# Optimization experiments

Measured on AMD Instinct MI355X. Metric: run time of the kernel, lower is better.

## Reference

```python
import jax, jax.numpy as jnp
import numpy as np

B, S, D, H, F = 4, 2048, 1024, 16, 4096
HD = D // H
NEG = -2.0 ** 32
EPS = 1e-5


def _gelu(x):
    return x * 0.5 * (1.0 + jax.scipy.special.erf(x / jnp.sqrt(2.0).astype(x.dtype)))


def _layernorm(x, scale, offset):
    mu = jnp.mean(x, axis=-1, keepdims=True)
    var = jnp.mean(jnp.square(x - mu), axis=-1, keepdims=True)
    return (x - mu) * jax.lax.rsqrt(var + EPS) * scale + offset


def setup_inputs() -> dict:
    key = jax.random.key(0)
    ks = jax.random.split(key, 12)
    s = 0.02
    return {
        "x": jax.random.normal(ks[0], (B, S, D), jnp.float32),
        "mask": jnp.zeros((B, S), jnp.int32),  # 1 = masked-out (padding)
        "Wq": jax.random.normal(ks[1], (D, D), jnp.float32) * s,
        "bq": jnp.zeros((D,), jnp.float32),
        "Wk": jax.random.normal(ks[2], (D, D), jnp.float32) * s,
        "bk": jnp.zeros((D,), jnp.float32),
        "Wv": jax.random.normal(ks[3], (D, D), jnp.float32) * s,
        "bv": jnp.zeros((D,), jnp.float32),
        "Wo": jax.random.normal(ks[4], (D, D), jnp.float32) * s,
        "bo": jnp.zeros((D,), jnp.float32),
        "ln1_s": jnp.ones((D,), jnp.float32),
        "ln1_b": jnp.zeros((D,), jnp.float32),
        "W1": jax.random.normal(ks[5], (D, F), jnp.float32) * s,
        "b1": jnp.zeros((F,), jnp.float32),
        "W2": jax.random.normal(ks[6], (F, D), jnp.float32) * s,
        "b2": jnp.zeros((D,), jnp.float32),
        "ln2_s": jnp.ones((D,), jnp.float32),
        "ln2_b": jnp.zeros((D,), jnp.float32),
    }


def reference(x, mask, Wq, bq, Wk, bk, Wv, bv, Wo, bo, ln1_s, ln1_b,
              W1, b1, W2, b2, ln2_s, ln2_b):
    b, s, d = x.shape
    q = (x @ Wq + bq).reshape(b, s, H, HD)
    k = (x @ Wk + bk).reshape(b, s, H, HD)
    v = (x @ Wv + bv).reshape(b, s, H, HD)
    logits = jnp.einsum('btnh,bsnh->bnts', q, k) / jnp.sqrt(jnp.float32(HD))
    logits = logits + (mask.astype(jnp.float32) * NEG)[:, None, None, :]
    attn = jax.nn.softmax(logits, axis=-1)
    ctx = jnp.einsum('bsnh,bnts->btnh', v, attn).reshape(b, s, d)
    attn_out = ctx @ Wo + bo
    h = _layernorm(attn_out + x, ln1_s, ln1_b)
    mlp = _gelu(h @ W1 + b1) @ W2 + b2
    return _layernorm(mlp + h, ln2_s, ln2_b)
```

## Files before the change

kernel.cpp:

```cpp
#include <hip/hip_runtime.h>
#include <hip/hip_bf16.h>

typedef __attribute__((ext_vector_type(8))) short short8;
typedef __attribute__((ext_vector_type(4))) short s16x4;
typedef __attribute__((ext_vector_type(4))) float f32x4;
typedef unsigned short u16;

#define DEV __device__ __forceinline__
#define MFMA32(a, b, c) __builtin_amdgcn_mfma_f32_16x16x32_bf16(a, b, c, 0, 0, 0)
#define MFMA16(a, b, c) __builtin_amdgcn_mfma_f32_16x16x16bf16_1k(a, b, c, 0, 0, 0)

DEV u16 f2b(float f) {
    __hip_bfloat16 h = __float2bfloat16(f);
    return __builtin_bit_cast(unsigned short, h);
}

DEV float max3f(float a, float b, float c) {
    float d;
    asm("v_max3_f32 %0, %1, %2, %3" : "=v"(d) : "v"(a), "v"(b), "v"(c));
    return d;
}

DEV void gl_lds16(const u16* g, u16* l) {
    __builtin_amdgcn_global_load_lds((const unsigned int*)g, (unsigned int*)l, 16, 0, 0);
}

__global__ __launch_bounds__(256) void cast_bf16(const float* __restrict__ in, u16* __restrict__ out, int n) {
    int i = (blockIdx.x * 256 + threadIdx.x) * 4;
    if (i < n) {
        float4 v = *(const float4*)(in + i);
        ushort4 o;
        o.x = f2b(v.x); o.y = f2b(v.y); o.z = f2b(v.z); o.w = f2b(v.w);
        *(ushort4*)(out + i) = o;
    }
}

__global__ __launch_bounds__(256) void transpose_cast(const float* __restrict__ in, u16* __restrict__ out,
                                                      int R, int C) {
    __shared__ float t[32][33];
    int bx = blockIdx.x * 32;
    int by = blockIdx.y * 32;
    int tx = threadIdx.x, ty = threadIdx.y;
#pragma unroll
    for (int i = 0; i < 32; i += 8) t[ty + i][tx] = in[(size_t)(by + ty + i) * C + bx + tx];
    __syncthreads();
#pragma unroll
    for (int i = 0; i < 32; i += 8) out[(size_t)(bx + ty + i) * R + by + tx] = f2b(t[tx][ty + i]);
}

__global__ __launch_bounds__(256) void pack_bias(const float* __restrict__ bq, const float* __restrict__ bk,
                                                 const float* __restrict__ bv, const float* __restrict__ bo,
                                                 const float* __restrict__ b1, const float* __restrict__ b2,
                                                 float* __restrict__ out) {
    int i = blockIdx.x * 256 + threadIdx.x;
    if (i >= 9216) return;
    float v;
    if (i < 1024) v = bq[i];
    else if (i < 2048) v = bk[i - 1024];
    else if (i < 3072) v = bv[i - 2048];
    else if (i < 4096) v = bo[i - 3072];
    else if (i < 8192) v = b1[i - 4096];
    else v = b2[i - 8192];
    out[i] = v;
}

template <bool GELU, bool BF16OUT, bool RESID>
__global__ __launch_bounds__(256) void gemm_bt(const u16* __restrict__ A, const u16* __restrict__ B,
                                               const float* __restrict__ bias, float* __restrict__ cf,
                                               u16* __restrict__ cb, const float* __restrict__ res,
                                               int M, int N, int K) {
    __shared__ __align__(16) u16 As[128 * 32];
    __shared__ __align__(16) u16 Bs[128 * 32];
    const int tid = threadIdx.x;
    const int wid = tid >> 6, lane = tid & 63;
    const int wr = wid >> 1, wc = wid & 1;
    const int m0 = blockIdx.x * 128, n0 = blockIdx.y * 128;
    const int r16 = lane & 15, g = lane >> 4;
    const int lrow = lane >> 2, lk = (lane & 3) * 8;

    f32x4 acc[4][4];
#pragma unroll
    for (int i = 0; i < 4; i++)
#pragma unroll
        for (int j = 0; j < 4; j++) acc[i][j] = (f32x4){0.f, 0.f, 0.f, 0.f};

    const u16* ga = A + (size_t)(m0 + wid * 32 + lrow) * K + lk;
    const u16* gb = B + (size_t)(n0 + wid * 32 + lrow) * K + lk;
    u16* lA0 = &As[(wid * 32) * 32];
    u16* lA1 = &As[(wid * 32 + 16) * 32];
    u16* lB0 = &Bs[(wid * 32) * 32];
    u16* lB1 = &Bs[(wid * 32 + 16) * 32];

    for (int kt = 0; kt < K; kt += 32) {
        gl_lds16(ga + kt, lA0);
        gl_lds16(ga + (size_t)16 * K + kt, lA1);
        gl_lds16(gb + kt, lB0);
        gl_lds16(gb + (size_t)16 * K + kt, lB1);
        __syncthreads();
        short8 af[4], bfr[4];
#pragma unroll
        for (int i = 0; i < 4; i++) af[i] = *(const short8*)&As[(wr * 64 + i * 16 + r16) * 32 + g * 8];
#pragma unroll
        for (int j = 0; j < 4; j++) bfr[j] = *(const short8*)&Bs[(wc * 64 + j * 16 + r16) * 32 + g * 8];
#pragma unroll
        for (int i = 0; i < 4; i++)
#pragma unroll
            for (int j = 0; j < 4; j++) acc[i][j] = MFMA32(af[i], bfr[j], acc[i][j]);
        __syncthreads();
    }

#pragma unroll
    for (int i = 0; i < 4; i++) {
#pragma unroll
        for (int j = 0; j < 4; j++) {
#pragma unroll
            for (int r = 0; r < 4; r++) {
                int row = m0 + wr * 64 + i * 16 + g * 4 + r;
                int col = n0 + wc * 64 + j * 16 + r16;
                float v = acc[i][j][r] + bias[col];
                if (RESID) v += res[(size_t)row * N + col];
                if (GELU) v = 0.5f * v * (1.0f + erff(v * 0.70710678118654752f));
                if (BF16OUT) cb[(size_t)row * N + col] = f2b(v);
                else cf[(size_t)row * N + col] = v;
            }
        }
    }
}

__global__ __launch_bounds__(256) void attn_kernel(const u16* __restrict__ qkv, const int* __restrict__ mask,
                                                   u16* __restrict__ ctx) {
    const int tid = threadIdx.x, wid = tid >> 6, lane = tid & 63;
    const int r16 = lane & 15, g = lane >> 4;
    const int h = blockIdx.y, b = blockIdx.z;
    const size_t baserow = (size_t)b * 2048;
    const int q0 = blockIdx.x * 64;

    __shared__ __align__(16) u16 Ks[64 * 64];
    __shared__ __align__(16) u16 Vs[64 * 64];
    __shared__ unsigned tflags_sh;

    const float SCALE = 0.18033688011112042f;
    const float MNEG = -6.196328018e9f;
    const s16x4 ONES = {(short)0x3F80, (short)0x3F80, (short)0x3F80, (short)0x3F80};

    short8 qf0, qf1;
    {
        const u16* qp = qkv + (baserow + q0 + wid * 16 + r16) * 3072 + h * 64 + g * 8;
        qf0 = *(const short8*)qp;
        qf1 = *(const short8*)(qp + 32);
    }

    if (tid == 0) tflags_sh = 0;
    __syncthreads();
    for (int r = 0; r < 8; ++r) {
        int v = mask[baserow + r * 256 + tid];
        unsigned long long bal = __ballot(v != 0);
        if (bal != 0 && lane == 0) atomicOr(&tflags_sh, 1u << (r * 4 + wid));
    }

    const int L = lane;
    const int kchunk = (L & 7) ^ (L >> 3);
    const u16* kg0 = qkv + (baserow + wid * 16 + (L >> 3)) * 3072 + 1024 + h * 64 + kchunk * 8;
    const u16* kg1 = kg0 + (size_t)8 * 3072;
    u16* kl0 = &Ks[wid * 1024];
    u16* kl1 = &Ks[wid * 1024 + 512];
    const u16* vg0 = qkv + (baserow + wid * 16 + ((L & 31) >> 1)) * 3072 + 2048 + h * 64
                     + ((L >> 5) * 16 + (L & 1) * 8);
    const u16* vg1 = vg0 + 32;
    u16* vl0 = &Vs[wid * 1024];
    u16* vl1 = &Vs[wid * 1024 + 512];
    const unsigned vaddr = (unsigned)(unsigned long long)&Vs[0] + (unsigned)(r16 * 2 + g * 128);

    __syncthreads();
    const unsigned tfl = tflags_sh;

    f32x4 Ot[4];
#pragma unroll
    for (int dt = 0; dt < 4; dt++) Ot[dt] = (f32x4){0.f, 0.f, 0.f, 0.f};
    f32x4 Osum = (f32x4){0.f, 0.f, 0.f, 0.f};
    float mrun = -1e30f;

    for (int t = 0; t < 32; ++t) {
        const int kt = t * 64;
        const size_t go = (size_t)kt * 3072;
        gl_lds16(kg0 + go, kl0);
        gl_lds16(kg1 + go, kl1);
        gl_lds16(vg0 + go, vl0);
        gl_lds16(vg1 + go, vl1);
        __syncthreads();

        f32x4 z[4];
        __builtin_amdgcn_s_setprio(1);
#pragma unroll
        for (int tt = 0; tt < 4; tt++) {
            const int row = tt * 16 + r16;
            const int swz = row & 7;
            short8 a0 = *(const short8*)&Ks[row * 64 + ((g ^ swz) * 8)];
            short8 a1 = *(const short8*)&Ks[row * 64 + (((4 + g) ^ swz) * 8)];
            f32x4 zz = (f32x4){0.f, 0.f, 0.f, 0.f};
            zz = MFMA32(a0, qf0, zz);
            zz = MFMA32(a1, qf1, zz);
            z[tt] = zz;
        }
        __builtin_amdgcn_s_setprio(0);

        float m0 = max3f(z[0][0], z[0][1], z[0][2]);
        float m1 = max3f(z[0][3], z[1][0], z[1][1]);
        float m2 = max3f(z[1][2], z[1][3], z[2][0]);
        float m3 = max3f(z[2][1], z[2][2], z[2][3]);
        float m4 = max3f(z[3][0], z[3][1], z[3][2]);
        float zmax = fmaxf(max3f(m0, m1, m2), max3f(m3, m4, z[3][3]));
        zmax = fmaxf(zmax, __shfl_xor(zmax, 16));
        zmax = fmaxf(zmax, __shfl_xor(zmax, 32));
        float pmax = zmax * SCALE;

        if (!__all(pmax - mrun <= 11.5f)) {
            float mnew = fmaxf(mrun, pmax);
            float alpha = exp2f(mrun - mnew);
            mrun = mnew;
            Osum *= alpha;
#pragma unroll
            for (int dt = 0; dt < 4; dt++) Ot[dt] *= alpha;
        }

        s16x4 pb[4];
        const float negm = -mrun;
        if (__builtin_expect((tfl >> t) & 1u, 0)) {
            const int* mrow = mask + baserow + kt;
#pragma unroll
            for (int tt = 0; tt < 4; tt++) {
                float p[4];
#pragma unroll
                for (int j = 0; j < 4; j++) {
                    float mbj = mrow[tt * 16 + g * 4 + j] ? MNEG : 0.0f;
                    p[j] = exp2f(__builtin_fmaf(z[tt][j], SCALE, mbj + negm));
                }
                unsigned lo, hi;
                asm("v_cvt_pk_bf16_f32 %0, %1, %2" : "=v"(lo) : "v"(p[0]), "v"(p[1]));
                asm("v_cvt_pk_bf16_f32 %0, %1, %2" : "=v"(hi) : "v"(p[2]), "v"(p[3]));
                uint2 u; u.x = lo; u.y = hi;
                pb[tt] = __builtin_bit_cast(s16x4, u);
            }
        } else {
#pragma unroll
            for (int tt = 0; tt < 4; tt++) {
                float p0 = exp2f(__builtin_fmaf(z[tt][0], SCALE, negm));
                float p1 = exp2f(__builtin_fmaf(z[tt][1], SCALE, negm));
                float p2 = exp2f(__builtin_fmaf(z[tt][2], SCALE, negm));
                float p3 = exp2f(__builtin_fmaf(z[tt][3], SCALE, negm));
                unsigned lo, hi;
                asm("v_cvt_pk_bf16_f32 %0, %1, %2" : "=v"(lo) : "v"(p0), "v"(p1));
                asm("v_cvt_pk_bf16_f32 %0, %1, %2" : "=v"(hi) : "v"(p2), "v"(p3));
                uint2 u; u.x = lo; u.y = hi;
                pb[tt] = __builtin_bit_cast(s16x4, u);
            }
        }

        s16x4 vf[4][4];
#pragma unroll
        for (int tt = 0; tt < 4; tt++)
#pragma unroll
            for (int dt = 0; dt < 4; dt++)
                asm volatile("ds_read_b64_tr_b16 %0, %1"
                             : "=v"(vf[tt][dt])
                             : "v"(vaddr + (unsigned)((tt * 4 + dt) * 512)));
        asm volatile("s_waitcnt lgkmcnt(0)" ::: "memory");
        __builtin_amdgcn_sched_barrier(0);
        __builtin_amdgcn_s_setprio(1);
#pragma unroll
        for (int tt = 0; tt < 4; tt++) {
#pragma unroll
            for (int dt = 0; dt < 4; dt++) Ot[dt] = MFMA16(vf[tt][dt], pb[tt], Ot[dt]);
            Osum = MFMA16(ONES, pb[tt], Osum);
        }
        __builtin_amdgcn_s_setprio(0);
        __syncthreads();
    }

    const float rl = 1.0f / Osum[0];
    u16* cp = ctx + (baserow + q0 + wid * 16 + r16) * 1024 + h * 64 + g * 4;
#pragma unroll
    for (int dt = 0; dt < 4; dt++) {
        ushort4 o4;
        o4.x = f2b(Ot[dt][0] * rl);
        o4.y = f2b(Ot[dt][1] * rl);
        o4.z = f2b(Ot[dt][2] * rl);
        o4.w = f2b(Ot[dt][3] * rl);
        *(ushort4*)(cp + dt * 16) = o4;
    }
}

__global__ __launch_bounds__(256) void ln_kernel(const float* __restrict__ a, const float* __restrict__ res,
                                                 const float* __restrict__ gamma, const float* __restrict__ beta,
                                                 float* __restrict__ outf, u16* __restrict__ outb) {
    const int row = blockIdx.x, tid = threadIdx.x;
    const size_t base = (size_t)row * 1024 + tid * 4;
    float4 va = *(const float4*)(a + base);
    float x0 = va.x, x1 = va.y, x2 = va.z, x3 = va.w;
    if (res) {
        float4 vr = *(const float4*)(res + base);
        x0 += vr.x; x1 += vr.y; x2 += vr.z; x3 += vr.w;
    }
    float s = x0 + x1 + x2 + x3;
    float ss = x0 * x0 + x1 * x1 + x2 * x2 + x3 * x3;
#pragma unroll
    for (int m = 1; m < 64; m <<= 1) { s += __shfl_xor(s, m, 64); ss += __shfl_xor(ss, m, 64); }
    __shared__ float red[8];
    if ((tid & 63) == 0) { red[tid >> 6] = s; red[4 + (tid >> 6)] = ss; }
    __syncthreads();
    s = red[0] + red[1] + red[2] + red[3];
    ss = red[4] + red[5] + red[6] + red[7];
    float mu = s * (1.0f / 1024.0f);
    float var = ss * (1.0f / 1024.0f) - mu * mu;
    float rstd = rsqrtf(var + 1e-5f);
    float4 g4 = *(const float4*)(gamma + tid * 4);
    float4 b4 = *(const float4*)(beta + tid * 4);
    float y0 = (x0 - mu) * rstd * g4.x + b4.x;
    float y1 = (x1 - mu) * rstd * g4.y + b4.y;
    float y2 = (x2 - mu) * rstd * g4.z + b4.z;
    float y3 = (x3 - mu) * rstd * g4.w + b4.w;
    *(float4*)(outf + base) = make_float4(y0, y1, y2, y3);
    if (outb) {
        ushort4 ob;
        ob.x = f2b(y0); ob.y = f2b(y1); ob.z = f2b(y2); ob.w = f2b(y3);
        *(ushort4*)(outb + base) = ob;
    }
}

extern "C" void kernel_launch(void* const* d_in, const int* in_sizes, int n_in, void* d_out, int out_size,
                              void* d_ws, size_t ws_size, hipStream_t stream) {
    const float* x = (const float*)d_in[0];
    const int* mask = (const int*)d_in[1];
    const float* Wq = (const float*)d_in[2];
    const float* bq = (const float*)d_in[3];
    const float* Wk = (const float*)d_in[4];
    const float* bk = (const float*)d_in[5];
    const float* Wv = (const float*)d_in[6];
    const float* bv = (const float*)d_in[7];
    const float* Wo = (const float*)d_in[8];
    const float* bo = (const float*)d_in[9];
    const float* ln1s = (const float*)d_in[10];
    const float* ln1b = (const float*)d_in[11];
    const float* W1 = (const float*)d_in[12];
    const float* b1 = (const float*)d_in[13];
    const float* W2 = (const float*)d_in[14];
    const float* b2 = (const float*)d_in[15];
    const float* ln2s = (const float*)d_in[16];
    const float* ln2b = (const float*)d_in[17];
    float* out = (float*)d_out;
    char* ws = (char*)d_ws;

    const size_t MB = 1024 * 1024;
    u16* XB = (u16*)(ws + 0);
    u16* WTq = (u16*)(ws + 16 * MB);
    u16* WTk = WTq + 1024 * 1024;
    u16* WTv = WTk + 1024 * 1024;
    u16* WTo = WTv + 1024 * 1024;
    u16* WT1 = WTo + 1024 * 1024;
    u16* WT2 = WT1 + 4096 * 1024;
    float* BIAS = (float*)(ws + 40 * MB);
    u16* QKV = (u16*)(ws + 41 * MB);
    u16* CTX = (u16*)(ws + 0);
    float* ATT = (float*)(ws + 41 * MB);
    float* Hbuf = (float*)(ws + 73 * MB);
    u16* HB = (u16*)(ws + 105 * MB);
    u16* MLP1 = (u16*)(ws + 121 * MB);
    float* MLP2 = (float*)(ws + 41 * MB);

    dim3 tb(32, 8);
    cast_bf16<<<8192, 256, 0, stream>>>(x, XB, 8192 * 1024);
    transpose_cast<<<dim3(32, 32), tb, 0, stream>>>(Wq, WTq, 1024, 1024);
    transpose_cast<<<dim3(32, 32), tb, 0, stream>>>(Wk, WTk, 1024, 1024);
    transpose_cast<<<dim3(32, 32), tb, 0, stream>>>(Wv, WTv, 1024, 1024);
    transpose_cast<<<dim3(32, 32), tb, 0, stream>>>(Wo, WTo, 1024, 1024);
    transpose_cast<<<dim3(128, 32), tb, 0, stream>>>(W1, WT1, 1024, 4096);
    transpose_cast<<<dim3(32, 128), tb, 0, stream>>>(W2, WT2, 4096, 1024);
    pack_bias<<<36, 256, 0, stream>>>(bq, bk, bv, bo, b1, b2, BIAS);

    gemm_bt<false, true, false><<<dim3(64, 24), 256, 0, stream>>>(XB, WTq, BIAS, nullptr, QKV, nullptr, 8192, 3072, 1024);
    attn_kernel<<<dim3(32, 16, 4), 256, 0, stream>>>(QKV, mask, CTX);
    gemm_bt<false, false, true><<<dim3(64, 8), 256, 0, stream>>>(CTX, WTo, BIAS + 3072, ATT, nullptr, x, 8192, 1024, 1024);
    ln_kernel<<<8192, 256, 0, stream>>>(ATT, nullptr, ln1s, ln1b, Hbuf, HB);
    gemm_bt<true, true, false><<<dim3(64, 32), 256, 0, stream>>>(HB, WT1, BIAS + 4096, nullptr, MLP1, nullptr, 8192, 4096, 1024);
    gemm_bt<false, false, true><<<dim3(64, 8), 256, 0, stream>>>(MLP1, WT2, BIAS + 8192, MLP2, nullptr, Hbuf, 8192, 1024, 4096);
    ln_kernel<<<8192, 256, 0, stream>>>(MLP2, nullptr, ln2s, ln2b, out, nullptr);
}
```

Before: 519.4 us.

## Process two query tiles per wave in attention to reuse K/V loads

Each attention block now covers 128 queries instead of 64, with every wave computing two 16-row query sub-tiles (A and B) that share the same K and V fragments read from shared memory. This halves the global K/V traffic and the block count, and amortizes LDS reads over twice the MFMA work. The V transpose reads are now double-buffered per key sub-tile and interleaved with the MFMAs rather than all issued up front. The cost is more registers per thread, constrained by the launch-bounds hint, and fewer blocks to fill the GPU.

```diff
diff --git a/kernel.cpp b/kernel.cpp
--- a/kernel.cpp
+++ b/kernel.cpp
@@ -127,13 +127,13 @@
     }
 }
 
-__global__ __launch_bounds__(256) void attn_kernel(const u16* __restrict__ qkv, const int* __restrict__ mask,
-                                                   u16* __restrict__ ctx) {
+__global__ __launch_bounds__(256, 4) void attn_kernel(const u16* __restrict__ qkv, const int* __restrict__ mask,
+                                                      u16* __restrict__ ctx) {
     const int tid = threadIdx.x, wid = tid >> 6, lane = tid & 63;
     const int r16 = lane & 15, g = lane >> 4;
     const int h = blockIdx.y, b = blockIdx.z;
     const size_t baserow = (size_t)b * 2048;
-    const int q0 = blockIdx.x * 64;
+    const int q0 = blockIdx.x * 128;
 
     __shared__ __align__(16) u16 Ks[64 * 64];
     __shared__ __align__(16) u16 Vs[64 * 64];
@@ -143,11 +143,13 @@
     const float MNEG = -6.196328018e9f;
     const s16x4 ONES = {(short)0x3F80, (short)0x3F80, (short)0x3F80, (short)0x3F80};
 
-    short8 qf0, qf1;
+    short8 qfA0, qfA1, qfB0, qfB1;
     {
-        const u16* qp = qkv + (baserow + q0 + wid * 16 + r16) * 3072 + h * 64 + g * 8;
-        qf0 = *(const short8*)qp;
-        qf1 = *(const short8*)(qp + 32);
+        const u16* qp = qkv + (baserow + q0 + wid * 32 + r16) * 3072 + h * 64 + g * 8;
+        qfA0 = *(const short8*)qp;
+        qfA1 = *(const short8*)(qp + 32);
+        qfB0 = *(const short8*)(qp + (size_t)16 * 3072);
+        qfB1 = *(const short8*)(qp + (size_t)16 * 3072 + 32);
     }
 
     if (tid == 0) tflags_sh = 0;
@@ -159,8 +161,7 @@
     }
 
     const int L = lane;
-    const int kchunk = (L & 7) ^ (L >> 3);
-    const u16* kg0 = qkv + (baserow + wid * 16 + (L >> 3)) * 3072 + 1024 + h * 64 + kchunk * 8;
+    const u16* kg0 = qkv + (baserow + wid * 16 + (L >> 3)) * 3072 + 1024 + h * 64 + ((L & 7) ^ (L >> 3)) * 8;
     const u16* kg1 = kg0 + (size_t)8 * 3072;
     u16* kl0 = &Ks[wid * 1024];
     u16* kl1 = &Ks[wid * 1024 + 512];
@@ -174,11 +175,11 @@
     __syncthreads();
     const unsigned tfl = tflags_sh;
 
-    f32x4 Ot[4];
-#pragma unroll
-    for (int dt = 0; dt < 4; dt++) Ot[dt] = (f32x4){0.f, 0.f, 0.f, 0.f};
-    f32x4 Osum = (f32x4){0.f, 0.f, 0.f, 0.f};
-    float mrun = -1e30f;
+    f32x4 OtA[4], OtB[4];
+#pragma unroll
+    for (int dt = 0; dt < 4; dt++) { OtA[dt] = (f32x4){0.f, 0.f, 0.f, 0.f}; OtB[dt] = (f32x4){0.f, 0.f, 0.f, 0.f}; }
+    f32x4 OsumA = (f32x4){0.f, 0.f, 0.f, 0.f}, OsumB = (f32x4){0.f, 0.f, 0.f, 0.f};
+    float mrunA = -1e30f, mrunB = -1e30f;
 
     for (int t = 0; t < 32; ++t) {
         const int kt = t * 64;
@@ -189,7 +190,7 @@
         gl_lds16(vg1 + go, vl1);
         __syncthreads();
 
-        f32x4 z[4];
+        f32x4 zA[4], zB[4];
         __builtin_amdgcn_s_setprio(1);
 #pragma unroll
         for (int tt = 0; tt < 4; tt++) {
@@ -197,96 +198,142 @@
             const int swz = row & 7;
             short8 a0 = *(const short8*)&Ks[row * 64 + ((g ^ swz) * 8)];
             short8 a1 = *(const short8*)&Ks[row * 64 + (((4 + g) ^ swz) * 8)];
-            f32x4 zz = (f32x4){0.f, 0.f, 0.f, 0.f};
-            zz = MFMA32(a0, qf0, zz);
-            zz = MFMA32(a1, qf1, zz);
-            z[tt] = zz;
+            f32x4 za = (f32x4){0.f, 0.f, 0.f, 0.f};
+            za = MFMA32(a0, qfA0, za);
+            za = MFMA32(a1, qfA1, za);
+            zA[tt] = za;
+            f32x4 zb = (f32x4){0.f, 0.f, 0.f, 0.f};
+            zb = MFMA32(a0, qfB0, zb);
+            zb = MFMA32(a1, qfB1, zb);
+            zB[tt] = zb;
         }
         __builtin_amdgcn_s_setprio(0);
 
-        float m0 = max3f(z[0][0], z[0][1], z[0][2]);
-        float m1 = max3f(z[0][3], z[1][0], z[1][1]);
-        float m2 = max3f(z[1][2], z[1][3], z[2][0]);
-        float m3 = max3f(z[2][1], z[2][2], z[2][3]);
-        float m4 = max3f(z[3][0], z[3][1], z[3][2]);
-        float zmax = fmaxf(max3f(m0, m1, m2), max3f(m3, m4, z[3][3]));
-        zmax = fmaxf(zmax, __shfl_xor(zmax, 16));
-        zmax = fmaxf(zmax, __shfl_xor(zmax, 32));
-        float pmax = zmax * SCALE;
-
-        if (!__all(pmax - mrun <= 11.5f)) {
-            float mnew = fmaxf(mrun, pmax);
-            float alpha = exp2f(mrun - mnew);
-            mrun = mnew;
-            Osum *= alpha;
-#pragma unroll
-            for (int dt = 0; dt < 4; dt++) Ot[dt] *= alpha;
-        }
-
-        s16x4 pb[4];
-        const float negm = -mrun;
+        float a0_ = max3f(zA[0][0], zA[0][1], zA[0][2]);
+        float a1_ = max3f(zA[0][3], zA[1][0], zA[1][1]);
+        float a2_ = max3f(zA[1][2], zA[1][3], zA[2][0]);
+        float a3_ = max3f(zA[2][1], zA[2][2], zA[2][3]);
+        float a4_ = max3f(zA[3][0], zA[3][1], zA[3][2]);
+        float zmaxA = fmaxf(max3f(a0_, a1_, a2_), max3f(a3_, a4_, zA[3][3]));
+        float b0_ = max3f(zB[0][0], zB[0][1], zB[0][2]);
+        float b1_ = max3f(zB[0][3], zB[1][0], zB[1][1]);
+        float b2_ = max3f(zB[1][2], zB[1][3], zB[2][0]);
+        float b3_ = max3f(zB[2][1], zB[2][2], zB[2][3]);
+        float b4_ = max3f(zB[3][0], zB[3][1], zB[3][2]);
+        float zmaxB = fmaxf(max3f(b0_, b1_, b2_), max3f(b3_, b4_, zB[3][3]));
+        zmaxA = fmaxf(zmaxA, __shfl_xor(zmaxA, 16));
+        zmaxB = fmaxf(zmaxB, __shfl_xor(zmaxB, 16));
+        zmaxA = fmaxf(zmaxA, __shfl_xor(zmaxA, 32));
+        zmaxB = fmaxf(zmaxB, __shfl_xor(zmaxB, 32));
+        float pmaxA = zmaxA * SCALE, pmaxB = zmaxB * SCALE;
+
+        if (!__all(pmaxA - mrunA <= 11.5f)) {
+            float mnew = fmaxf(mrunA, pmaxA);
+            float alpha = exp2f(mrunA - mnew);
+            mrunA = mnew;
+            OsumA *= alpha;
+#pragma unroll
+            for (int dt = 0; dt < 4; dt++) OtA[dt] *= alpha;
+        }
+        if (!__all(pmaxB - mrunB <= 11.5f)) {
+            float mnew = fmaxf(mrunB, pmaxB);
+            float alpha = exp2f(mrunB - mnew);
+            mrunB = mnew;
+            OsumB *= alpha;
+#pragma unroll
+            for (int dt = 0; dt < 4; dt++) OtB[dt] *= alpha;
+        }
+
+        s16x4 pbA[4], pbB[4];
+        const float negmA = -mrunA, negmB = -mrunB;
         if (__builtin_expect((tfl >> t) & 1u, 0)) {
             const int* mrow = mask + baserow + kt;
 #pragma unroll
             for (int tt = 0; tt < 4; tt++) {
-                float p[4];
+                float pa[4], pbv[4];
 #pragma unroll
                 for (int j = 0; j < 4; j++) {
                     float mbj = mrow[tt * 16 + g * 4 + j] ? MNEG : 0.0f;
-                    p[j] = exp2f(__builtin_fmaf(z[tt][j], SCALE, mbj + negm));
+                    pa[j] = exp2f(__builtin_fmaf(zA[tt][j], SCALE, mbj + negmA));
+                    pbv[j] = exp2f(__builtin_fmaf(zB[tt][j], SCALE, mbj + negmB));
                 }
                 unsigned lo, hi;
-                asm("v_cvt_pk_bf16_f32 %0, %1, %2" : "=v"(lo) : "v"(p[0]), "v"(p[1]));
-                asm("v_cvt_pk_bf16_f32 %0, %1, %2" : "=v"(hi) : "v"(p[2]), "v"(p[3]));
-                uint2 u; u.x = lo; u.y = hi;
-                pb[tt] = __builtin_bit_cast(s16x4, u);
+                asm("v_cvt_pk_bf16_f32 %0, %1, %2" : "=v"(lo) : "v"(pa[0]), "v"(pa[1]));
+                asm("v_cvt_pk_bf16_f32 %0, %1, %2" : "=v"(hi) : "v"(pa[2]), "v"(pa[3]));
+                uint2 ua; ua.x = lo; ua.y = hi;
+                pbA[tt] = __builtin_bit_cast(s16x4, ua);
+                asm("v_cvt_pk_bf16_f32 %0, %1, %2" : "=v"(lo) : "v"(pbv[0]), "v"(pbv[1]));
+                asm("v_cvt_pk_bf16_f32 %0, %1, %2" : "=v"(hi) : "v"(pbv[2]), "v"(pbv[3]));
+                uint2 ub; ub.x = lo; ub.y = hi;
+                pbB[tt] = __builtin_bit_cast(s16x4, ub);
             }
         } else {
 #pragma unroll
             for (int tt = 0; tt < 4; tt++) {
-                float p0 = exp2f(__builtin_fmaf(z[tt][0], SCALE, negm));
-                float p1 = exp2f(__builtin_fmaf(z[tt][1], SCALE, negm));
-                float p2 = exp2f(__builtin_fmaf(z[tt][2], SCALE, negm));
-                float p3 = exp2f(__builtin_fmaf(z[tt][3], SCALE, negm));
+                float pa0 = exp2f(__builtin_fmaf(zA[tt][0], SCALE, negmA));
+                float pa1 = exp2f(__builtin_fmaf(zA[tt][1], SCALE, negmA));
+                float pa2 = exp2f(__builtin_fmaf(zA[tt][2], SCALE, negmA));
+                float pa3 = exp2f(__builtin_fmaf(zA[tt][3], SCALE, negmA));
+                float pb0 = exp2f(__builtin_fmaf(zB[tt][0], SCALE, negmB));
+                float pb1 = exp2f(__builtin_fmaf(zB[tt][1], SCALE, negmB));
+                float pb2 = exp2f(__builtin_fmaf(zB[tt][2], SCALE, negmB));
+                float pb3 = exp2f(__builtin_fmaf(zB[tt][3], SCALE, negmB));
                 unsigned lo, hi;
-                asm("v_cvt_pk_bf16_f32 %0, %1, %2" : "=v"(lo) : "v"(p0), "v"(p1));
-                asm("v_cvt_pk_bf16_f32 %0, %1, %2" : "=v"(hi) : "v"(p2), "v"(p3));
-                uint2 u; u.x = lo; u.y = hi;
-                pb[tt] = __builtin_bit_cast(s16x4, u);
+                asm("v_cvt_pk_bf16_f32 %0, %1, %2" : "=v"(lo) : "v"(pa0), "v"(pa1));
+                asm("v_cvt_pk_bf16_f32 %0, %1, %2" : "=v"(hi) : "v"(pa2), "v"(pa3));
+                uint2 ua; ua.x = lo; ua.y = hi;
+                pbA[tt] = __builtin_bit_cast(s16x4, ua);
+                asm("v_cvt_pk_bf16_f32 %0, %1, %2" : "=v"(lo) : "v"(pb0), "v"(pb1));
+                asm("v_cvt_pk_bf16_f32 %0, %1, %2" : "=v"(hi) : "v"(pb2), "v"(pb3));
+                uint2 ub; ub.x = lo; ub.y = hi;
+                pbB[tt] = __builtin_bit_cast(s16x4, ub);
             }
         }
 
-        s16x4 vf[4][4];
-#pragma unroll
-        for (int tt = 0; tt < 4; tt++)
-#pragma unroll
-            for (int dt = 0; dt < 4; dt++)
-                asm volatile("ds_read_b64_tr_b16 %0, %1"
-                             : "=v"(vf[tt][dt])
-                             : "v"(vaddr + (unsigned)((tt * 4 + dt) * 512)));
-        asm volatile("s_waitcnt lgkmcnt(0)" ::: "memory");
-        __builtin_amdgcn_sched_barrier(0);
-        __builtin_amdgcn_s_setprio(1);
+        s16x4 vf[2][4];
+#pragma unroll
+        for (int dt = 0; dt < 4; dt++)
+            asm volatile("ds_read_b64_tr_b16 %0, %1"
+                         : "=v"(vf[0][dt]) : "v"(vaddr + (unsigned)(dt * 512)));
 #pragma unroll
         for (int tt = 0; tt < 4; tt++) {
-#pragma unroll
-            for (int dt = 0; dt < 4; dt++) Ot[dt] = MFMA16(vf[tt][dt], pb[tt], Ot[dt]);
-            Osum = MFMA16(ONES, pb[tt], Osum);
-        }
-        __builtin_amdgcn_s_setprio(0);
+            if (tt < 3) {
+#pragma unroll
+                for (int dt = 0; dt < 4; dt++)
+                    asm volatile("ds_read_b64_tr_b16 %0, %1"
+                                 : "=v"(vf[(tt + 1) & 1][dt])
+                                 : "v"(vaddr + (unsigned)(((tt + 1) * 4 + dt) * 512)));
+                asm volatile("s_waitcnt lgkmcnt(4)" ::: "memory");
+            } else {
+                asm volatile("s_waitcnt lgkmcnt(0)" ::: "memory");
+            }
+            __builtin_amdgcn_sched_barrier(0);
+            __builtin_amdgcn_s_setprio(1);
+#pragma unroll
+            for (int dt = 0; dt < 4; dt++) {
+                OtA[dt] = MFMA16(vf[tt & 1][dt], pbA[tt], OtA[dt]);
+                OtB[dt] = MFMA16(vf[tt & 1][dt], pbB[tt], OtB[dt]);
+            }
+            OsumA = MFMA16(ONES, pbA[tt], OsumA);
+            OsumB = MFMA16(ONES, pbB[tt], OsumB);
+            __builtin_amdgcn_s_setprio(0);
+        }
         __syncthreads();
     }
 
-    const float rl = 1.0f / Osum[0];
-    u16* cp = ctx + (baserow + q0 + wid * 16 + r16) * 1024 + h * 64 + g * 4;
+    const float rlA = 1.0f / OsumA[0];
+    const float rlB = 1.0f / OsumB[0];
+    u16* cpA = ctx + (baserow + q0 + wid * 32 + r16) * 1024 + h * 64 + g * 4;
+    u16* cpB = cpA + (size_t)16 * 1024;
 #pragma unroll
     for (int dt = 0; dt < 4; dt++) {
-        ushort4 o4;
-        o4.x = f2b(Ot[dt][0] * rl);
-        o4.y = f2b(Ot[dt][1] * rl);
-        o4.z = f2b(Ot[dt][2] * rl);
-        o4.w = f2b(Ot[dt][3] * rl);
-        *(ushort4*)(cp + dt * 16) = o4;
+        ushort4 oa, ob;
+        oa.x = f2b(OtA[dt][0] * rlA); oa.y = f2b(OtA[dt][1] * rlA);
+        oa.z = f2b(OtA[dt][2] * rlA); oa.w = f2b(OtA[dt][3] * rlA);
+        ob.x = f2b(OtB[dt][0] * rlB); ob.y = f2b(OtB[dt][1] * rlB);
+        ob.z = f2b(OtB[dt][2] * rlB); ob.w = f2b(OtB[dt][3] * rlB);
+        *(ushort4*)(cpA + dt * 16) = oa;
+        *(ushort4*)(cpB + dt * 16) = ob;
     }
 }
 
@@ -378,7 +425,7 @@
     pack_bias<<<36, 256, 0, stream>>>(bq, bk, bv, bo, b1, b2, BIAS);
 
     gemm_bt<false, true, false><<<dim3(64, 24), 256, 0, stream>>>(XB, WTq, BIAS, nullptr, QKV, nullptr, 8192, 3072, 1024);
-    attn_kernel<<<dim3(32, 16, 4), 256, 0, stream>>>(QKV, mask, CTX);
+    attn_kernel<<<dim3(16, 16, 4), 256, 0, stream>>>(QKV, mask, CTX);
     gemm_bt<false, false, true><<<dim3(64, 8), 256, 0, stream>>>(CTX, WTo, BIAS + 3072, ATT, nullptr, x, 8192, 1024, 1024);
     ln_kernel<<<8192, 256, 0, stream>>>(ATT, nullptr, ln1s, ln1b, Hbuf, HB);
     gemm_bt<true, true, false><<<dim3(64, 32), 256, 0, stream>>>(HB, WT1, BIAS + 4096, nullptr, MLP1, nullptr, 8192, 4096, 1024);
```

Measured after the change: 518.3 us. About the same (-0.2%).
